# Optimization experiments

Hardware: AMD Instinct MI355X
Metric: run time of the kernel (lower is better)

## Reference

```python
import jax, jax.numpy as jnp
import numpy as np

N = 100000      # nodes
E = 1_600_000   # edges (avg degree 16)
D = 64          # input_dim
H = 64          # hidden_dim
OUT = 40        # output_dim (classes)


def setup_inputs() -> dict:
    key = jax.random.key(0)
    ks = jax.random.split(key, 12)

    def glorot(k, shape):
        lim = float(np.sqrt(6.0 / (shape[0] + shape[1])))
        return jax.random.uniform(k, shape, jnp.float32, -lim, lim)

    return {
        "x": jax.random.normal(ks[0], (N, D), jnp.float32),
        "edge_index": jax.random.randint(ks[1], (2, E), 0, N, dtype=jnp.int32),
        "batch": jnp.zeros((N,), jnp.int32),  # unused for task='node'
        "W0": glorot(ks[2], (D, H)),  "b0": jnp.zeros((H,), jnp.float32),
        "W1": glorot(ks[3], (H, H)),  "b1": jnp.zeros((H,), jnp.float32),
        "W2": glorot(ks[4], (H, H)),  "b2": jnp.zeros((H,), jnp.float32),
        "Wp1": glorot(ks[5], (H, H // 2)), "bp1": jnp.zeros((H // 2,), jnp.float32),
        "Wp2": glorot(ks[6], (H // 2, OUT)), "bp2": jnp.zeros((OUT,), jnp.float32),
    }


def gcn_conv(x, src, dst, W, b):
    """PyG GCNConv: x' = D^{-1/2}(A+I)D^{-1/2} (x W) + b, self-loop weight 1."""
    n = x.shape[0]
    h = x @ W                                      # [N, H] dense transform first
    loops = jnp.arange(n, dtype=src.dtype)
    src2 = jnp.concatenate([src, loops])           # add self loops
    dst2 = jnp.concatenate([dst, loops])
    deg = jax.ops.segment_sum(jnp.ones_like(dst2, h.dtype), dst2, num_segments=n)
    dinv = jnp.where(deg > 0, jax.lax.rsqrt(deg), 0.0)
    norm = dinv[src2] * dinv[dst2]                 # [E+N]
    # gather-scale-scatter: messages from source nodes aggregated at dest
    out = jax.ops.segment_sum(h[src2] * norm[:, None], dst2, num_segments=n)
    return out + b


def reference(x, edge_index, batch, W0, b0, W1, b1, W2, b2, Wp1, bp1, Wp2, bp2):
    src, dst = edge_index[0], edge_index[1]
    for W, b in ((W0, b0), (W1, b1), (W2, b2)):
        x = jax.nn.relu(gcn_conv(x, src, dst, W, b))
        # dropout is identity in inference mode
    # post_mp MLP head
    x = jax.nn.relu(x @ Wp1 + bp1) @ Wp2 + bp2
    return jax.nn.log_softmax(x, axis=1)
```

## Files before the change

### kernel.cpp

```cpp
#include <hip/hip_runtime.h>
#include <hip/hip_bf16.h>
#include <math.h>


#define DIMF 64
#define NBA  200
#define BSH  9

static __device__ __forceinline__ unsigned short f2bf(float f)
{
    __hip_bfloat16 b = __float2bfloat16(f);
    return *(unsigned short*)&b;
}


__global__ __launch_bounds__(256) void bucket_count(
    const int* __restrict__ dst, int* __restrict__ partial, int E, int tile)
{
    __shared__ int h[256];
    int t = threadIdx.x;
    h[t] = 0;
    __syncthreads();
    int estart = blockIdx.x * tile;
    int eend = min(E, estart + tile);
    for (int e = estart + t; e < eend; e += 256)
        atomicAdd(&h[dst[e] >> BSH], 1);
    __syncthreads();
    partial[blockIdx.x * 256 + t] = h[t];
}

__global__ __launch_bounds__(256) void bucket_scan(
    const int* __restrict__ partial, int* __restrict__ bucket_off,
    int* __restrict__ gcursor, int nba)
{
    __shared__ int s[256];
    int t = threadIdx.x;
    int sum = 0;
    for (int b = 0; b < nba; b++) sum += partial[b * 256 + t];
    s[t] = sum;
    __syncthreads();
    for (int off = 1; off < 256; off <<= 1) {
        int v = (t >= off) ? s[t - off] : 0;
        __syncthreads();
        s[t] += v;
        __syncthreads();
    }
    int excl = s[t] - sum;
    bucket_off[t] = excl;
    gcursor[t] = excl;
    if (t == 255) bucket_off[256] = s[t];
}

__global__ __launch_bounds__(256) void bucket_scatter(
    const int* __restrict__ src, const int* __restrict__ dst,
    const int* __restrict__ partial, int* __restrict__ gcursor,
    unsigned int* __restrict__ ebuf, int E, int tile)
{
    __shared__ int h[256];
    int t = threadIdx.x;
    h[t] = atomicAdd(&gcursor[t], partial[blockIdx.x * 256 + t]);
    __syncthreads();
    int estart = blockIdx.x * tile;
    int eend = min(E, estart + tile);
    for (int e = estart + t; e < eend; e += 256) {
        int d = dst[e];
        int p = atomicAdd(&h[d >> BSH], 1);
        ebuf[p] = ((unsigned int)src[e] << BSH) | (unsigned int)(d & 511);
    }
}

__global__ __launch_bounds__(256) void bucket_csr(
    const unsigned int* __restrict__ ebuf, const int* __restrict__ bucket_off,
    int* __restrict__ row_start, int* __restrict__ csr_src,
    float* __restrict__ dinv, int n, int E)
{
    __shared__ int cnt[512];
    __shared__ int ps[256];
    int t = threadIdx.x;
    int blk = blockIdx.x;
    int node0 = blk << BSH;
    cnt[t] = 0; cnt[t + 256] = 0;
    __syncthreads();
    int bs = bucket_off[blk], be = bucket_off[blk + 1];
    for (int i = bs + t; i < be; i += 256)
        atomicAdd(&cnt[ebuf[i] & 511], 1);
    __syncthreads();
    int c0 = cnt[2 * t], c1 = cnt[2 * t + 1];
    ps[t] = c0 + c1;
    __syncthreads();
    for (int off = 1; off < 256; off <<= 1) {
        int v = (t >= off) ? ps[t - off] : 0;
        __syncthreads();
        ps[t] += v;
        __syncthreads();
    }
    int pexcl = ps[t] - (c0 + c1);
    int e0 = pexcl, e1 = pexcl + c0;
    int g0 = node0 + 2 * t, g1 = g0 + 1;
    if (g0 < n) { row_start[g0] = bs + e0; dinv[g0] = rsqrtf((float)c0 + 1.0f); }
    if (g1 < n) { row_start[g1] = bs + e1; dinv[g1] = rsqrtf((float)c1 + 1.0f); }
    __syncthreads();
    cnt[2 * t] = e0; cnt[2 * t + 1] = e1;
    __syncthreads();
    for (int i = bs + t; i < be; i += 256) {
        unsigned int pk = ebuf[i];
        int p = bs + atomicAdd(&cnt[pk & 511], 1);
        csr_src[p] = (int)(pk >> BSH);
    }
    if (blk == gridDim.x - 1 && t == 0) row_start[n] = E;
}


#define GEMM_RB(ACC0, ACC1, XS, WS)                                        \
    float ACC0[4] = {0.f, 0.f, 0.f, 0.f};                                  \
    float ACC1[4] = {0.f, 0.f, 0.f, 0.f};                                  \
    {                                                                      \
        int cg4 = (t & 15) << 2;                                           \
        int rr0 = (t >> 4) << 1;                                           \
        _Pragma("unroll 4")                                                \
        for (int k = 0; k < 64; k++) {                                     \
            float4 w = *(const float4*)&WS[(k << 6) + cg4];                \
            float x0 = XS[rr0][k];                                         \
            float x1 = XS[rr0 + 1][k];                                     \
            ACC0[0] = fmaf(x0, w.x, ACC0[0]);                              \
            ACC0[1] = fmaf(x0, w.y, ACC0[1]);                              \
            ACC0[2] = fmaf(x0, w.z, ACC0[2]);                              \
            ACC0[3] = fmaf(x0, w.w, ACC0[3]);                              \
            ACC1[0] = fmaf(x1, w.x, ACC1[0]);                              \
            ACC1[1] = fmaf(x1, w.y, ACC1[1]);                              \
            ACC1[2] = fmaf(x1, w.z, ACC1[2]);                              \
            ACC1[3] = fmaf(x1, w.w, ACC1[3]);                              \
        }                                                                  \
    }

#define GEMM_STORE(ACC, GR)                                                \
    if ((GR) < n) {                                                        \
        float dv = dinv[GR];                                               \
        ushort4 u;                                                         \
        u.x = f2bf(ACC[0] * dv);                                           \
        u.y = f2bf(ACC[1] * dv);                                           \
        u.z = f2bf(ACC[2] * dv);                                           \
        u.w = f2bf(ACC[3] * dv);                                           \
        *(ushort4*)(hpout + (size_t)(GR) * DIMF + ((t & 15) << 2)) = u;    \
    }

#define ZERO_ROW(HP)                                                       \
    if (blockIdx.x == 0 && t < 32)                                         \
        ((unsigned int*)(HP))[(size_t)n * 32 + t] = 0u;


__global__ __launch_bounds__(256) void gemm_scale_f32(
    const float* __restrict__ xin, const float* __restrict__ W,
    const float* __restrict__ dinv, __hip_bfloat16* __restrict__ hpout, int n)
{
    __shared__ float Ws[64 * 64];
    __shared__ float Xs[32][65];
    int t = threadIdx.x;
    ZERO_ROW(hpout)
    {
        const float4* Wv = (const float4*)W;
        float4* Wsv = (float4*)Ws;
        for (int i = t; i < 1024; i += 256) Wsv[i] = Wv[i];
    }
    int row0 = blockIdx.x * 32;
    for (int i = t; i < 512; i += 256) {
        int r = i >> 4, c4 = (i & 15) << 2;
        int gr = row0 + r;
        float4 v = {0.f, 0.f, 0.f, 0.f};
        if (gr < n) v = *(const float4*)(xin + (size_t)gr * DIMF + c4);
        Xs[r][c4]     = v.x;
        Xs[r][c4 + 1] = v.y;
        Xs[r][c4 + 2] = v.z;
        Xs[r][c4 + 3] = v.w;
    }
    __syncthreads();

    GEMM_RB(acc0, acc1, Xs, Ws)
    int gr0 = row0 + ((t >> 4) << 1);
    GEMM_STORE(acc0, gr0)
    GEMM_STORE(acc1, gr0 + 1)
}


#define ADDROW(a, v)                                                       \
    {                                                                      \
        a[0] += __uint_as_float((v).x << 16);                              \
        a[1] += __uint_as_float((v).x & 0xffff0000u);                      \
        a[2] += __uint_as_float((v).y << 16);                              \
        a[3] += __uint_as_float((v).y & 0xffff0000u);                      \
        a[4] += __uint_as_float((v).z << 16);                              \
        a[5] += __uint_as_float((v).z & 0xffff0000u);                      \
        a[6] += __uint_as_float((v).w << 16);                              \
        a[7] += __uint_as_float((v).w & 0xffff0000u);                      \
    }

#define GIDX(DST, J)                                                       \
    {                                                                      \
        int _t = csr_src[rs + (J)];                                        \
        DST = ((J) < deg) ? _t : n;                                        \
    }

#define GATHER_BODY(xv_out)                                                    \
    float xv_out[8];                                                           \
    {                                                                          \
        int rs = row_start[node];                                              \
        int deg = row_start[node + 1] - rs;                                    \
        float a0[8], a1[8], a2[8], a3[8];                                      \
        _Pragma("unroll")                                                      \
        for (int i = 0; i < 8; i++) { a0[i]=0.f; a1[i]=0.f; a2[i]=0.f; a3[i]=0.f; } \
        {                                                                      \
            uint4 v = *(const uint4*)(hprime + (size_t)node * 32 + uoff);      \
            ADDROW(a0, v);                                                     \
        }                                                                      \
        int i0, i1, i2, i3, i4, i5, i6, i7;                                    \
        GIDX(i0, 0) GIDX(i1, 1) GIDX(i2, 2) GIDX(i3, 3)                        \
        GIDX(i4, 4) GIDX(i5, 5) GIDX(i6, 6) GIDX(i7, 7)                        \
        for (int k = 0; k < deg; k += 8) {                                     \
            int kn = k + 8;                                                    \
            int m0, m1, m2, m3, m4, m5, m6, m7;                                \
            GIDX(m0, kn + 0) GIDX(m1, kn + 1) GIDX(m2, kn + 2) GIDX(m3, kn + 3)\
            GIDX(m4, kn + 4) GIDX(m5, kn + 5) GIDX(m6, kn + 6) GIDX(m7, kn + 7)\
            uint4 v0 = *(const uint4*)(hprime + (size_t)i0 * 32 + uoff);       \
            uint4 v1 = *(const uint4*)(hprime + (size_t)i1 * 32 + uoff);       \
            uint4 v2 = *(const uint4*)(hprime + (size_t)i2 * 32 + uoff);       \
            uint4 v3 = *(const uint4*)(hprime + (size_t)i3 * 32 + uoff);       \
            uint4 v4 = *(const uint4*)(hprime + (size_t)i4 * 32 + uoff);       \
            uint4 v5 = *(const uint4*)(hprime + (size_t)i5 * 32 + uoff);       \
            uint4 v6 = *(const uint4*)(hprime + (size_t)i6 * 32 + uoff);       \
            uint4 v7 = *(const uint4*)(hprime + (size_t)i7 * 32 + uoff);       \
            ADDROW(a0, v0); ADDROW(a1, v1); ADDROW(a2, v2); ADDROW(a3, v3);    \
            ADDROW(a0, v4); ADDROW(a1, v5); ADDROW(a2, v6); ADDROW(a3, v7);    \
            i0 = m0; i1 = m1; i2 = m2; i3 = m3;                                \
            i4 = m4; i5 = m5; i6 = m6; i7 = m7;                                \
        }                                                                      \
        int f8 = uoff << 1;                                                    \
        float dv = dinv[node];                                                 \
        _Pragma("unroll")                                                      \
        for (int j = 0; j < 8; j++)                                            \
            xv_out[j] = fmaxf(fmaf(dv, a0[j] + a1[j] + a2[j] + a3[j],          \
                                   b[f8 + j]), 0.0f);                          \
    }


__global__ __launch_bounds__(256) void gather_gemm(
    const unsigned int* __restrict__ hprime,
    const int* __restrict__ row_start, const int* __restrict__ csr_src,
    const float* __restrict__ dinv, const float* __restrict__ b,
    const float* __restrict__ Wn,
    __hip_bfloat16* __restrict__ hpout, int n)
{
    __shared__ float Ws[64 * 64];
    __shared__ float Xs[32][65];
    int t = threadIdx.x;
    ZERO_ROW(hpout)
    {
        const float4* Wv = (const float4*)Wn;
        float4* Wsv = (float4*)Ws;
        for (int i = t; i < 1024; i += 256) Wsv[i] = Wv[i];
    }

    int wave = t >> 6;
    int lane = t & 63;
    int slot = lane >> 3;
    int o    = lane & 7;
    int uoff = o << 2;
    int ln   = (wave << 3) + slot;
    int row0 = blockIdx.x * 32;
    int node = row0 + ln;
    int f8l  = o << 3;

    if (node < n) {
        GATHER_BODY(xv)
#pragma unroll
        for (int j = 0; j < 8; j++) Xs[ln][f8l + j] = xv[j];
    } else {
#pragma unroll
        for (int j = 0; j < 8; j++) Xs[ln][f8l + j] = 0.0f;
    }
    __syncthreads();

    GEMM_RB(acc0, acc1, Xs, Ws)
    int gr0 = row0 + ((t >> 4) << 1);
    GEMM_STORE(acc0, gr0)
    GEMM_STORE(acc1, gr0 + 1)
}


__global__ __launch_bounds__(256) void gather_head(
    const unsigned int* __restrict__ hprime,
    const int* __restrict__ row_start, const int* __restrict__ csr_src,
    const float* __restrict__ dinv, const float* __restrict__ b,
    const float* __restrict__ Wp1, const float* __restrict__ bp1,
    const float* __restrict__ Wp2, const float* __restrict__ bp2,
    float* __restrict__ out, int n)
{
    __shared__ float W1s[64 * 32];
    __shared__ float W2t[40][36];
    __shared__ float b1s[32], b2s[40];
    __shared__ float Xs[32][65];
    __shared__ float Hs[32][33];
    int t = threadIdx.x;
    {
        const float4* Wv = (const float4*)Wp1;
        float4* Wsv = (float4*)W1s;
        for (int i = t; i < 512; i += 256) Wsv[i] = Wv[i];
    }
    for (int i = t; i < 1280; i += 256) {
        int k = i & 31, j = i >> 5;
        W2t[j][k] = Wp2[k * 40 + j];
    }
    if (t < 32) b1s[t] = bp1[t];
    if (t < 40) b2s[t] = bp2[t];

    int wave = t >> 6;
    int lane = t & 63;
    int slot = lane >> 3;
    int o    = lane & 7;
    int uoff = o << 2;
    int ln   = (wave << 3) + slot;
    int node = blockIdx.x * 32 + ln;
    int f8l  = o << 3;

    if (node < n) {
        GATHER_BODY(xv)
#pragma unroll
        for (int j = 0; j < 8; j++) Xs[ln][f8l + j] = xv[j];
    } else {
#pragma unroll
        for (int j = 0; j < 8; j++) Xs[ln][f8l + j] = 0.0f;
    }
    __syncthreads();

    float h[4];
#pragma unroll
    for (int m = 0; m < 4; m++) h[m] = b1s[o * 4 + m];
#pragma unroll 4
    for (int k = 0; k < 64; k++) {
        float xk = Xs[ln][k];
        float4 w = *(const float4*)&W1s[(k << 5) + (o << 2)];
        h[0] = fmaf(xk, w.x, h[0]);
        h[1] = fmaf(xk, w.y, h[1]);
        h[2] = fmaf(xk, w.z, h[2]);
        h[3] = fmaf(xk, w.w, h[3]);
    }
#pragma unroll
    for (int m = 0; m < 4; m++) Hs[ln][o * 4 + m] = fmaxf(h[m], 0.0f);

    if (node < n) {
        float oo[5];
#pragma unroll
        for (int m = 0; m < 5; m++) oo[m] = b2s[o * 5 + m];
#pragma unroll
        for (int k4 = 0; k4 < 8; k4++) {
            float hk0 = Hs[ln][4 * k4 + 0];
            float hk1 = Hs[ln][4 * k4 + 1];
            float hk2 = Hs[ln][4 * k4 + 2];
            float hk3 = Hs[ln][4 * k4 + 3];
#pragma unroll
            for (int m = 0; m < 5; m++) {
                float4 w = *(const float4*)&W2t[o * 5 + m][4 * k4];
                oo[m] = fmaf(hk3, w.w, fmaf(hk2, w.z,
                         fmaf(hk1, w.y, fmaf(hk0, w.x, oo[m]))));
            }
        }
        float mx = oo[0];
#pragma unroll
        for (int m = 1; m < 5; m++) mx = fmaxf(mx, oo[m]);
#pragma unroll
        for (int mask = 1; mask <= 4; mask <<= 1) mx = fmaxf(mx, __shfl_xor(mx, mask));
        float se = 0.0f;
#pragma unroll
        for (int m = 0; m < 5; m++) se += expf(oo[m] - mx);
#pragma unroll
        for (int mask = 1; mask <= 4; mask <<= 1) se += __shfl_xor(se, mask);
        float lse = logf(se) + mx;
        float* op = out + (size_t)node * 40 + o * 5;
#pragma unroll
        for (int m = 0; m < 5; m++) op[m] = oo[m] - lse;
    }
}

extern "C" void kernel_launch(void* const* d_in, const int* in_sizes, int n_in,
                              void* d_out, int out_size, void* d_ws, size_t ws_size,
                              hipStream_t stream)
{
    const float* x  = (const float*)d_in[0];
    const int*   ei = (const int*)d_in[1];
    const int E = in_sizes[1] / 2;
    const int n = in_sizes[0] / DIMF;
    const int* src = ei;
    const int* dst = ei + E;
    const float* W0 = (const float*)d_in[3];  const float* b0 = (const float*)d_in[4];
    const float* W1 = (const float*)d_in[5];  const float* b1 = (const float*)d_in[6];
    const float* W2 = (const float*)d_in[7];  const float* b2 = (const float*)d_in[8];
    const float* Wp1 = (const float*)d_in[9];  const float* bp1 = (const float*)d_in[10];
    const float* Wp2 = (const float*)d_in[11]; const float* bp2 = (const float*)d_in[12];
    float* out = (float*)d_out;

    const int NBK  = (n + 511) >> BSH;
    const int tile = (E + NBA - 1) / NBA;

#define ALIGN256(q) (char*)(((size_t)(q) + 255) & ~(size_t)255)
    char* p = (char*)d_ws;
    int* partial    = (int*)p;                p += (size_t)NBA * 256 * 4;
    p = ALIGN256(p);
    int* bucket_off = (int*)p;                p += 257 * 4;
    p = ALIGN256(p);
    int* gcursor    = (int*)p;                p += 256 * 4;
    p = ALIGN256(p);
    int* row_start  = (int*)p;                p += (size_t)(n + 1) * 4;
    p = ALIGN256(p);
    float* dinv     = (float*)p;              p += (size_t)n * 4;
    p = ALIGN256(p);
    int* csr_src    = (int*)p;                p += (size_t)E * 4;
    p = ALIGN256(p);
    __hip_bfloat16* hpA = (__hip_bfloat16*)p; p += (size_t)(n + 1) * DIMF * 2;
    p = ALIGN256(p);
    __hip_bfloat16* hpB = (__hip_bfloat16*)p;
    unsigned int* ebuf  = (unsigned int*)hpB;

    const int nblk = (n + 31) / 32;

    hipLaunchKernelGGL(bucket_count,   dim3(NBA), dim3(256), 0, stream, dst, partial, E, tile);
    hipLaunchKernelGGL(bucket_scan,    dim3(1),   dim3(256), 0, stream, partial, bucket_off, gcursor, NBA);
    hipLaunchKernelGGL(bucket_scatter, dim3(NBA), dim3(256), 0, stream, src, dst, partial, gcursor, ebuf, E, tile);
    hipLaunchKernelGGL(bucket_csr,     dim3(NBK), dim3(256), 0, stream, ebuf, bucket_off,
                       row_start, csr_src, dinv, n, E);

    hipLaunchKernelGGL(gemm_scale_f32, dim3(nblk), dim3(256), 0, stream,
                       x, W0, dinv, hpA, n);
    hipLaunchKernelGGL(gather_gemm, dim3(nblk), dim3(256), 0, stream,
                       (const unsigned int*)hpA, row_start, csr_src, dinv, b0,
                       W1, hpB, n);
    hipLaunchKernelGGL(gather_gemm, dim3(nblk), dim3(256), 0, stream,
                       (const unsigned int*)hpB, row_start, csr_src, dinv, b1,
                       W2, hpA, n);
    hipLaunchKernelGGL(gather_head, dim3(nblk), dim3(256), 0, stream,
                       (const unsigned int*)hpA, row_start, csr_src, dinv, b2,
                       Wp1, bp1, Wp2, bp2, out, n);
}
```

Before: 320.7 us.

## Make gather_gemm persistent and overlap next tile's gather with current GEMM

gather_gemm becomes a grid-stride persistent kernel capped at 1024 blocks. Each iteration interleaves the neighbor gather loads for the next tile with 16-k chunks of the current tile's GEMM, so gather latency hides behind FMA work. Sentinel entries (row_start[n+1], dinv[n]) are added so tail threads can clamp to node n without branching. This costs higher register pressure and extra barriers per tile, and fewer blocks in flight for latency hiding.

```diff
diff --git a/kernel.cpp b/kernel.cpp
--- a/kernel.cpp
+++ b/kernel.cpp
@@ -6,6 +6,7 @@
 #define DIMF 64
 #define NBA  200
 #define BSH  9
+#define GGRID 1024
 
 static __device__ __forceinline__ unsigned short f2bf(float f)
 {
@@ -107,30 +108,25 @@
         int p = bs + atomicAdd(&cnt[pk & 511], 1);
         csr_src[p] = (int)(pk >> BSH);
     }
-    if (blk == gridDim.x - 1 && t == 0) row_start[n] = E;
-}
-
-
-#define GEMM_RB(ACC0, ACC1, XS, WS)                                        \
-    float ACC0[4] = {0.f, 0.f, 0.f, 0.f};                                  \
-    float ACC1[4] = {0.f, 0.f, 0.f, 0.f};                                  \
-    {                                                                      \
-        int cg4 = (t & 15) << 2;                                           \
-        int rr0 = (t >> 4) << 1;                                           \
-        _Pragma("unroll 4")                                                \
-        for (int k = 0; k < 64; k++) {                                     \
-            float4 w = *(const float4*)&WS[(k << 6) + cg4];                \
-            float x0 = XS[rr0][k];                                         \
-            float x1 = XS[rr0 + 1][k];                                     \
-            ACC0[0] = fmaf(x0, w.x, ACC0[0]);                              \
-            ACC0[1] = fmaf(x0, w.y, ACC0[1]);                              \
-            ACC0[2] = fmaf(x0, w.z, ACC0[2]);                              \
-            ACC0[3] = fmaf(x0, w.w, ACC0[3]);                              \
-            ACC1[0] = fmaf(x1, w.x, ACC1[0]);                              \
-            ACC1[1] = fmaf(x1, w.y, ACC1[1]);                              \
-            ACC1[2] = fmaf(x1, w.z, ACC1[2]);                              \
-            ACC1[3] = fmaf(x1, w.w, ACC1[3]);                              \
-        }                                                                  \
+    if (blk == gridDim.x - 1 && t == 0) {
+        row_start[n] = E;
+        row_start[n + 1] = E;
+        dinv[n] = 0.0f;
+    }
+}
+
+
+#define GEMM_CHUNK(KB)                                                      \
+    _Pragma("unroll")                                                       \
+    for (int kk = 0; kk < 16; kk++) {                                       \
+        int k = (KB) + kk;                                                  \
+        float4 w = *(const float4*)&Ws[(k << 6) + cg4];                     \
+        float x0 = Xs[rr0][k];                                              \
+        float x1 = Xs[rr0 + 1][k];                                          \
+        acc0[0] = fmaf(x0, w.x, acc0[0]); acc0[1] = fmaf(x0, w.y, acc0[1]); \
+        acc0[2] = fmaf(x0, w.z, acc0[2]); acc0[3] = fmaf(x0, w.w, acc0[3]); \
+        acc1[0] = fmaf(x1, w.x, acc1[0]); acc1[1] = fmaf(x1, w.y, acc1[1]); \
+        acc1[2] = fmaf(x1, w.z, acc1[2]); acc1[3] = fmaf(x1, w.w, acc1[3]); \
     }
 
 #define GEMM_STORE(ACC, GR)                                                \
@@ -175,8 +171,12 @@
     }
     __syncthreads();
 
-    GEMM_RB(acc0, acc1, Xs, Ws)
-    int gr0 = row0 + ((t >> 4) << 1);
+    int cg4 = (t & 15) << 2;
+    int rr0 = (t >> 4) << 1;
+    float acc0[4] = {0.f, 0.f, 0.f, 0.f};
+    float acc1[4] = {0.f, 0.f, 0.f, 0.f};
+    GEMM_CHUNK(0) GEMM_CHUNK(16) GEMM_CHUNK(32) GEMM_CHUNK(48)
+    int gr0 = row0 + rr0;
     GEMM_STORE(acc0, gr0)
     GEMM_STORE(acc1, gr0 + 1)
 }
@@ -242,12 +242,42 @@
     }
 
 
+#define G_ISSUE(C)                                                          \
+    act = (C) < gs;                                                         \
+    if (act) {                                                              \
+        rv0 = *(const uint4*)(hprime + (size_t)gi0 * 32 + uoff);            \
+        rv1 = *(const uint4*)(hprime + (size_t)gi1 * 32 + uoff);            \
+        rv2 = *(const uint4*)(hprime + (size_t)gi2 * 32 + uoff);            \
+        rv3 = *(const uint4*)(hprime + (size_t)gi3 * 32 + uoff);            \
+        rv4 = *(const uint4*)(hprime + (size_t)gi4 * 32 + uoff);            \
+        rv5 = *(const uint4*)(hprime + (size_t)gi5 * 32 + uoff);            \
+        rv6 = *(const uint4*)(hprime + (size_t)gi6 * 32 + uoff);            \
+        rv7 = *(const uint4*)(hprime + (size_t)gi7 * 32 + uoff);            \
+        int kn = ((C) + 1) << 3;                                            \
+        q0 = csr_src[rs + kn + 0]; q1 = csr_src[rs + kn + 1];               \
+        q2 = csr_src[rs + kn + 2]; q3 = csr_src[rs + kn + 3];               \
+        q4 = csr_src[rs + kn + 4]; q5 = csr_src[rs + kn + 5];               \
+        q6 = csr_src[rs + kn + 6]; q7 = csr_src[rs + kn + 7];               \
+    }
+
+#define G_CONSUME(C)                                                        \
+    if (act) {                                                              \
+        ADDROW(a0, rv0); ADDROW(a1, rv1); ADDROW(a2, rv2); ADDROW(a3, rv3); \
+        ADDROW(a0, rv4); ADDROW(a1, rv5); ADDROW(a2, rv6); ADDROW(a3, rv7); \
+        int kn = ((C) + 1) << 3;                                            \
+        gi0 = (kn + 0 < deg) ? q0 : n; gi1 = (kn + 1 < deg) ? q1 : n;       \
+        gi2 = (kn + 2 < deg) ? q2 : n; gi3 = (kn + 3 < deg) ? q3 : n;       \
+        gi4 = (kn + 4 < deg) ? q4 : n; gi5 = (kn + 5 < deg) ? q5 : n;       \
+        gi6 = (kn + 6 < deg) ? q6 : n; gi7 = (kn + 7 < deg) ? q7 : n;       \
+    }
+
+
 __global__ __launch_bounds__(256) void gather_gemm(
     const unsigned int* __restrict__ hprime,
     const int* __restrict__ row_start, const int* __restrict__ csr_src,
     const float* __restrict__ dinv, const float* __restrict__ b,
     const float* __restrict__ Wn,
-    __hip_bfloat16* __restrict__ hpout, int n)
+    __hip_bfloat16* __restrict__ hpout, int n, int ntiles)
 {
     __shared__ float Ws[64 * 64];
     __shared__ float Xs[32][65];
@@ -265,24 +295,102 @@
     int o    = lane & 7;
     int uoff = o << 2;
     int ln   = (wave << 3) + slot;
-    int row0 = blockIdx.x * 32;
-    int node = row0 + ln;
     int f8l  = o << 3;
-
-    if (node < n) {
-        GATHER_BODY(xv)
+    int cg4  = (t & 15) << 2;
+    int rr0  = (t >> 4) << 1;
+
+    int tile = blockIdx.x;
+    if (tile >= ntiles) return;
+
+    float xv[8];
+    {
+        int node = tile * 32 + ln;
+        if (node < n) {
+            GATHER_BODY(xvp)
+#pragma unroll
+            for (int j = 0; j < 8; j++) xv[j] = xvp[j];
+        } else {
+#pragma unroll
+            for (int j = 0; j < 8; j++) xv[j] = 0.0f;
+        }
+    }
+
+    while (true) {
+        int row0 = tile * 32;
+        int ntile = tile + (int)gridDim.x;
+
+        int nn = min(ntile * 32 + ln, n);
+        int rs  = row_start[nn];
+        int re  = row_start[nn + 1];
+        float dvn = dinv[nn];
+        uint4 vself = *(const uint4*)(hprime + (size_t)nn * 32 + uoff);
+
+        __syncthreads();
 #pragma unroll
         for (int j = 0; j < 8; j++) Xs[ln][f8l + j] = xv[j];
-    } else {
-#pragma unroll
-        for (int j = 0; j < 8; j++) Xs[ln][f8l + j] = 0.0f;
-    }
-    __syncthreads();
-
-    GEMM_RB(acc0, acc1, Xs, Ws)
-    int gr0 = row0 + ((t >> 4) << 1);
-    GEMM_STORE(acc0, gr0)
-    GEMM_STORE(acc1, gr0 + 1)
+        __syncthreads();
+
+        int deg = re - rs;
+        int gs  = (deg + 7) >> 3;
+        int gi0, gi1, gi2, gi3, gi4, gi5, gi6, gi7;
+        GIDX(gi0, 0) GIDX(gi1, 1) GIDX(gi2, 2) GIDX(gi3, 3)
+        GIDX(gi4, 4) GIDX(gi5, 5) GIDX(gi6, 6) GIDX(gi7, 7)
+
+        float a0[8], a1[8], a2[8], a3[8];
+#pragma unroll
+        for (int i = 0; i < 8; i++) { a0[i]=0.f; a1[i]=0.f; a2[i]=0.f; a3[i]=0.f; }
+        uint4 rv0, rv1, rv2, rv3, rv4, rv5, rv6, rv7;
+        int q0, q1, q2, q3, q4, q5, q6, q7;
+        bool act;
+
+        float acc0[4] = {0.f, 0.f, 0.f, 0.f};
+        float acc1[4] = {0.f, 0.f, 0.f, 0.f};
+
+        G_ISSUE(0)
+        ADDROW(a0, vself);
+        GEMM_CHUNK(0)
+        G_CONSUME(0)
+        G_ISSUE(1)
+        GEMM_CHUNK(16)
+        G_CONSUME(1)
+        G_ISSUE(2)
+        GEMM_CHUNK(32)
+        G_CONSUME(2)
+        G_ISSUE(3)
+        GEMM_CHUNK(48)
+        G_CONSUME(3)
+
+        for (int jr = 4; jr < gs; jr++) {
+            uint4 w0 = *(const uint4*)(hprime + (size_t)gi0 * 32 + uoff);
+            uint4 w1 = *(const uint4*)(hprime + (size_t)gi1 * 32 + uoff);
+            uint4 w2 = *(const uint4*)(hprime + (size_t)gi2 * 32 + uoff);
+            uint4 w3 = *(const uint4*)(hprime + (size_t)gi3 * 32 + uoff);
+            uint4 w4 = *(const uint4*)(hprime + (size_t)gi4 * 32 + uoff);
+            uint4 w5 = *(const uint4*)(hprime + (size_t)gi5 * 32 + uoff);
+            uint4 w6 = *(const uint4*)(hprime + (size_t)gi6 * 32 + uoff);
+            uint4 w7 = *(const uint4*)(hprime + (size_t)gi7 * 32 + uoff);
+            int kn = (jr + 1) << 3;
+            int p0, p1, p2, p3, p4, p5, p6, p7;
+            GIDX(p0, kn + 0) GIDX(p1, kn + 1) GIDX(p2, kn + 2) GIDX(p3, kn + 3)
+            GIDX(p4, kn + 4) GIDX(p5, kn + 5) GIDX(p6, kn + 6) GIDX(p7, kn + 7)
+            ADDROW(a0, w0); ADDROW(a1, w1); ADDROW(a2, w2); ADDROW(a3, w3);
+            ADDROW(a0, w4); ADDROW(a1, w5); ADDROW(a2, w6); ADDROW(a3, w7);
+            gi0 = p0; gi1 = p1; gi2 = p2; gi3 = p3;
+            gi4 = p4; gi5 = p5; gi6 = p6; gi7 = p7;
+        }
+
+#pragma unroll
+        for (int j = 0; j < 8; j++)
+            xv[j] = fmaxf(fmaf(dvn, a0[j] + a1[j] + a2[j] + a3[j],
+                               b[f8l + j]), 0.0f);
+
+        int gr0 = row0 + rr0;
+        GEMM_STORE(acc0, gr0)
+        GEMM_STORE(acc1, gr0 + 1)
+
+        if (ntile >= ntiles) break;
+        tile = ntile;
+    }
 }
 
 
@@ -408,9 +516,9 @@
     p = ALIGN256(p);
     int* gcursor    = (int*)p;                p += 256 * 4;
     p = ALIGN256(p);
-    int* row_start  = (int*)p;                p += (size_t)(n + 1) * 4;
-    p = ALIGN256(p);
-    float* dinv     = (float*)p;              p += (size_t)n * 4;
+    int* row_start  = (int*)p;                p += (size_t)(n + 2) * 4;
+    p = ALIGN256(p);
+    float* dinv     = (float*)p;              p += (size_t)(n + 1) * 4;
     p = ALIGN256(p);
     int* csr_src    = (int*)p;                p += (size_t)E * 4;
     p = ALIGN256(p);
@@ -420,6 +528,7 @@
     unsigned int* ebuf  = (unsigned int*)hpB;
 
     const int nblk = (n + 31) / 32;
+    const int ggrid = (nblk < GGRID) ? nblk : GGRID;
 
     hipLaunchKernelGGL(bucket_count,   dim3(NBA), dim3(256), 0, stream, dst, partial, E, tile);
     hipLaunchKernelGGL(bucket_scan,    dim3(1),   dim3(256), 0, stream, partial, bucket_off, gcursor, NBA);
@@ -429,12 +538,12 @@
 
     hipLaunchKernelGGL(gemm_scale_f32, dim3(nblk), dim3(256), 0, stream,
                        x, W0, dinv, hpA, n);
-    hipLaunchKernelGGL(gather_gemm, dim3(nblk), dim3(256), 0, stream,
+    hipLaunchKernelGGL(gather_gemm, dim3(ggrid), dim3(256), 0, stream,
                        (const unsigned int*)hpA, row_start, csr_src, dinv, b0,
-                       W1, hpB, n);
-    hipLaunchKernelGGL(gather_gemm, dim3(nblk), dim3(256), 0, stream,
+                       W1, hpB, n, nblk);
+    hipLaunchKernelGGL(gather_gemm, dim3(ggrid), dim3(256), 0, stream,
                        (const unsigned int*)hpB, row_start, csr_src, dinv, b1,
-                       W2, hpA, n);
+                       W2, hpA, n, nblk);
     hipLaunchKernelGGL(gather_head, dim3(nblk), dim3(256), 0, stream,
                        (const unsigned int*)hpA, row_start, csr_src, dinv, b2,
                        Wp1, bp1, Wp2, bp2, out, n);
```

After: 477.7 us. 48.9% more time.

## Sort nodes by degree and process gather kernels in degree-bucketed order

Applied to the files above, without the earlier changes.

Builds a degree histogram while constructing the CSR, then counting-sorts node ids into a permutation grouped by in-degree. The gather_gemm and gather_head kernels process nodes in permuted order, so each wave handles nodes of similar degree, which is meant to reduce divergence and load imbalance in the neighbour loops. This costs two extra small kernels and an indirection per node, and it scatters output rows so stores and dinv reads become non-contiguous.

```diff
diff --git a/kernel.cpp b/kernel.cpp
--- a/kernel.cpp
+++ b/kernel.cpp
@@ -31,10 +31,11 @@
 
 __global__ __launch_bounds__(256) void bucket_scan(
     const int* __restrict__ partial, int* __restrict__ bucket_off,
-    int* __restrict__ gcursor, int nba)
+    int* __restrict__ gcursor, int* __restrict__ ghist, int nba)
 {
     __shared__ int s[256];
     int t = threadIdx.x;
+    if (t < 64) ghist[t] = 0;
     int sum = 0;
     for (int b = 0; b < nba; b++) sum += partial[b * 256 + t];
     s[t] = sum;
@@ -72,14 +73,16 @@
 __global__ __launch_bounds__(256) void bucket_csr(
     const unsigned int* __restrict__ ebuf, const int* __restrict__ bucket_off,
     int* __restrict__ row_start, int* __restrict__ csr_src,
-    float* __restrict__ dinv, int n, int E)
+    float* __restrict__ dinv, int* __restrict__ ghist, int n, int E)
 {
     __shared__ int cnt[512];
     __shared__ int ps[256];
+    __shared__ int dh[64];
     int t = threadIdx.x;
     int blk = blockIdx.x;
     int node0 = blk << BSH;
     cnt[t] = 0; cnt[t + 256] = 0;
+    if (t < 64) dh[t] = 0;
     __syncthreads();
     int bs = bucket_off[blk], be = bucket_off[blk + 1];
     for (int i = bs + t; i < be; i += 256)
@@ -97,8 +100,14 @@
     int pexcl = ps[t] - (c0 + c1);
     int e0 = pexcl, e1 = pexcl + c0;
     int g0 = node0 + 2 * t, g1 = g0 + 1;
-    if (g0 < n) { row_start[g0] = bs + e0; dinv[g0] = rsqrtf((float)c0 + 1.0f); }
-    if (g1 < n) { row_start[g1] = bs + e1; dinv[g1] = rsqrtf((float)c1 + 1.0f); }
+    if (g0 < n) {
+        row_start[g0] = bs + e0; dinv[g0] = rsqrtf((float)c0 + 1.0f);
+        atomicAdd(&dh[min(c0, 63)], 1);
+    }
+    if (g1 < n) {
+        row_start[g1] = bs + e1; dinv[g1] = rsqrtf((float)c1 + 1.0f);
+        atomicAdd(&dh[min(c1, 63)], 1);
+    }
     __syncthreads();
     cnt[2 * t] = e0; cnt[2 * t + 1] = e1;
     __syncthreads();
@@ -107,7 +116,51 @@
         int p = bs + atomicAdd(&cnt[pk & 511], 1);
         csr_src[p] = (int)(pk >> BSH);
     }
+    if (t < 64 && dh[t]) atomicAdd(&ghist[t], dh[t]);
     if (blk == gridDim.x - 1 && t == 0) row_start[n] = E;
+}
+
+
+__global__ void deg_scan(const int* __restrict__ ghist, int* __restrict__ gdcur)
+{
+    __shared__ int s[64];
+    int t = threadIdx.x;
+    s[t] = ghist[t];
+    __syncthreads();
+    if (t == 0) {
+        int acc = 0;
+        for (int i = 0; i < 64; i++) { int v = s[i]; s[i] = acc; acc += v; }
+    }
+    __syncthreads();
+    gdcur[t] = s[t];
+}
+
+__global__ __launch_bounds__(256) void deg_scatter(
+    const int* __restrict__ row_start, int* __restrict__ gdcur,
+    int* __restrict__ perm, int n)
+{
+    __shared__ int lh[64];
+    __shared__ int lbase[64];
+    int t = threadIdx.x;
+    if (t < 64) lh[t] = 0;
+    __syncthreads();
+    int i0 = blockIdx.x * 512;
+    int iend = min(n, i0 + 512);
+    for (int i = i0 + t; i < iend; i += 256) {
+        int d = min(row_start[i + 1] - row_start[i], 63);
+        atomicAdd(&lh[d], 1);
+    }
+    __syncthreads();
+    if (t < 64) {
+        lbase[t] = lh[t] ? atomicAdd(&gdcur[t], lh[t]) : 0;
+        lh[t] = 0;
+    }
+    __syncthreads();
+    for (int i = i0 + t; i < iend; i += 256) {
+        int d = min(row_start[i + 1] - row_start[i], 63);
+        int off = atomicAdd(&lh[d], 1);
+        perm[lbase[d] + off] = i;
+    }
 }
 
 
@@ -142,6 +195,18 @@
         u.z = f2bf(ACC[2] * dv);                                           \
         u.w = f2bf(ACC[3] * dv);                                           \
         *(ushort4*)(hpout + (size_t)(GR) * DIMF + ((t & 15) << 2)) = u;    \
+    }
+
+#define GEMM_STORE_P(ACC, GI)                                              \
+    if ((GI) < n) {                                                        \
+        int pr = perm[GI];                                                 \
+        float dv = dinv[pr];                                               \
+        ushort4 u;                                                         \
+        u.x = f2bf(ACC[0] * dv);                                           \
+        u.y = f2bf(ACC[1] * dv);                                           \
+        u.z = f2bf(ACC[2] * dv);                                           \
+        u.w = f2bf(ACC[3] * dv);                                           \
+        *(ushort4*)(hpout + (size_t)pr * DIMF + ((t & 15) << 2)) = u;      \
     }
 
 #define ZERO_ROW(HP)                                                       \
@@ -247,6 +312,7 @@
     const int* __restrict__ row_start, const int* __restrict__ csr_src,
     const float* __restrict__ dinv, const float* __restrict__ b,
     const float* __restrict__ Wn,
+    const int* __restrict__ perm,
     __hip_bfloat16* __restrict__ hpout, int n)
 {
     __shared__ float Ws[64 * 64];
@@ -266,10 +332,11 @@
     int uoff = o << 2;
     int ln   = (wave << 3) + slot;
     int row0 = blockIdx.x * 32;
-    int node = row0 + ln;
+    int gidx = row0 + ln;
     int f8l  = o << 3;
 
-    if (node < n) {
+    if (gidx < n) {
+        int node = perm[gidx];
         GATHER_BODY(xv)
 #pragma unroll
         for (int j = 0; j < 8; j++) Xs[ln][f8l + j] = xv[j];
@@ -280,9 +347,9 @@
     __syncthreads();
 
     GEMM_RB(acc0, acc1, Xs, Ws)
-    int gr0 = row0 + ((t >> 4) << 1);
-    GEMM_STORE(acc0, gr0)
-    GEMM_STORE(acc1, gr0 + 1)
+    int g0i = row0 + ((t >> 4) << 1);
+    GEMM_STORE_P(acc0, g0i)
+    GEMM_STORE_P(acc1, g0i + 1)
 }
 
 
@@ -292,6 +359,7 @@
     const float* __restrict__ dinv, const float* __restrict__ b,
     const float* __restrict__ Wp1, const float* __restrict__ bp1,
     const float* __restrict__ Wp2, const float* __restrict__ bp2,
+    const int* __restrict__ perm,
     float* __restrict__ out, int n)
 {
     __shared__ float W1s[64 * 32];
@@ -318,10 +386,12 @@
     int o    = lane & 7;
     int uoff = o << 2;
     int ln   = (wave << 3) + slot;
-    int node = blockIdx.x * 32 + ln;
+    int gidx = blockIdx.x * 32 + ln;
+    int node = n;
     int f8l  = o << 3;
 
-    if (node < n) {
+    if (gidx < n) {
+        node = perm[gidx];
         GATHER_BODY(xv)
 #pragma unroll
         for (int j = 0; j < 8; j++) Xs[ln][f8l + j] = xv[j];
@@ -346,7 +416,7 @@
 #pragma unroll
     for (int m = 0; m < 4; m++) Hs[ln][o * 4 + m] = fmaxf(h[m], 0.0f);
 
-    if (node < n) {
+    if (gidx < n) {
         float oo[5];
 #pragma unroll
         for (int m = 0; m < 5; m++) oo[m] = b2s[o * 5 + m];
@@ -408,6 +478,12 @@
     p = ALIGN256(p);
     int* gcursor    = (int*)p;                p += 256 * 4;
     p = ALIGN256(p);
+    int* ghist      = (int*)p;                p += 64 * 4;
+    p = ALIGN256(p);
+    int* gdcur      = (int*)p;                p += 64 * 4;
+    p = ALIGN256(p);
+    int* perm       = (int*)p;                p += (size_t)n * 4;
+    p = ALIGN256(p);
     int* row_start  = (int*)p;                p += (size_t)(n + 1) * 4;
     p = ALIGN256(p);
     float* dinv     = (float*)p;              p += (size_t)n * 4;
@@ -420,22 +496,25 @@
     unsigned int* ebuf  = (unsigned int*)hpB;
 
     const int nblk = (n + 31) / 32;
+    const int NBD  = (n + 511) / 512;
 
     hipLaunchKernelGGL(bucket_count,   dim3(NBA), dim3(256), 0, stream, dst, partial, E, tile);
-    hipLaunchKernelGGL(bucket_scan,    dim3(1),   dim3(256), 0, stream, partial, bucket_off, gcursor, NBA);
+    hipLaunchKernelGGL(bucket_scan,    dim3(1),   dim3(256), 0, stream, partial, bucket_off, gcursor, ghist, NBA);
     hipLaunchKernelGGL(bucket_scatter, dim3(NBA), dim3(256), 0, stream, src, dst, partial, gcursor, ebuf, E, tile);
     hipLaunchKernelGGL(bucket_csr,     dim3(NBK), dim3(256), 0, stream, ebuf, bucket_off,
-                       row_start, csr_src, dinv, n, E);
+                       row_start, csr_src, dinv, ghist, n, E);
+    hipLaunchKernelGGL(deg_scan,       dim3(1),   dim3(64),  0, stream, ghist, gdcur);
+    hipLaunchKernelGGL(deg_scatter,    dim3(NBD), dim3(256), 0, stream, row_start, gdcur, perm, n);
 
     hipLaunchKernelGGL(gemm_scale_f32, dim3(nblk), dim3(256), 0, stream,
                        x, W0, dinv, hpA, n);
     hipLaunchKernelGGL(gather_gemm, dim3(nblk), dim3(256), 0, stream,
                        (const unsigned int*)hpA, row_start, csr_src, dinv, b0,
-                       W1, hpB, n);
+                       W1, perm, hpB, n);
     hipLaunchKernelGGL(gather_gemm, dim3(nblk), dim3(256), 0, stream,
                        (const unsigned int*)hpB, row_start, csr_src, dinv, b1,
-                       W2, hpA, n);
+                       W2, perm, hpA, n);
     hipLaunchKernelGGL(gather_head, dim3(nblk), dim3(256), 0, stream,
                        (const unsigned int*)hpA, row_start, csr_src, dinv, b2,
-                       Wp1, bp1, Wp2, bp2, out, n);
-}
+                       Wp1, bp1, Wp2, bp2, perm, out, n);
+}
```

Measured after the change: 329.8 us. +2.8%, slower.
